# Optimization experiments

Measured on AMD Instinct MI355X. Metric: run time of the kernel, lower is better.

The kernel has to match this reference:

```python
import jax, jax.numpy as jnp
import numpy as np

L, D, H, G, HS, I, V, B, T = 4, 1024, 16, 4, 64, 2816, 32000, 4, 512
THETA = 10000.0
EPS = 1e-6


def setup_inputs() -> dict:
    key = jax.random.key(0)
    ks = jax.random.split(key, 10)
    s = 0.02
    return {
        "input_ids": jax.random.randint(ks[0], (B, T), 0, V),
        "embed": jax.random.normal(ks[1], (V, D)) * s,      # tied with lm_head
        "q_w": jax.random.normal(ks[2], (L, D, D)) * s,     # torch Linear: [out, in]
        "q_b": jax.random.normal(ks[3], (L, D)) * s,
        "kv_w": jax.random.normal(ks[4], (L, 2 * G * HS, D)) * s,
        "kv_b": jax.random.normal(ks[5], (L, 2 * G * HS)) * s,
        "o_w": jax.random.normal(ks[6], (L, D, D)) * s,
        "ln1_w": jnp.ones((L, D)),
        "ln2_w": jnp.ones((L, D)),
        "gate_w": jax.random.normal(ks[7], (L, I, D)) * s,
        "up_w": jax.random.normal(ks[8], (L, I, D)) * s,
        "down_w": jax.random.normal(ks[9], (L, D, I)) * s,
        "last_w": jnp.ones((D,)),
    }


def rms_norm(x, w):
    return x * jax.lax.rsqrt(jnp.mean(x * x, axis=-1, keepdims=True) + EPS) * w


def rope_tables(t, hs):
    inv_freq = 1.0 / (THETA ** (jnp.arange(0, hs, 2, dtype=jnp.float32) / hs))
    ang = jnp.arange(t, dtype=jnp.float32)[:, None] * inv_freq[None, :]  # [T, hs/2]
    emb = jnp.concatenate([ang, ang], axis=-1)                           # [T, hs]
    return jnp.cos(emb), jnp.sin(emb)


def rotate_half(x):
    x1, x2 = jnp.split(x, 2, axis=-1)
    return jnp.concatenate([-x2, x1], axis=-1)


def reference(input_ids, embed, q_w, q_b, kv_w, kv_b, o_w, ln1_w, ln2_w, gate_w, up_w, down_w, last_w):
    x = embed[input_ids]  # [B, T, D]
    cos, sin = rope_tables(T, HS)                    # [T, HS] (buffers, const)
    c, s_ = cos[None, None], sin[None, None]         # [1, 1, T, HS]
    causal = jnp.tril(jnp.ones((T, T), dtype=bool))
    scale = 1.0 / np.sqrt(HS).astype(np.float32)
    for l in range(L):
        h = rms_norm(x, ln1_w[l])
        q = (h @ q_w[l].T + q_b[l]).reshape(B, T, H, HS).transpose(0, 2, 1, 3)  # bhtd
        kv = h @ kv_w[l].T + kv_b[l]
        k, v = jnp.split(kv, 2, axis=-1)
        k = k.reshape(B, T, G, HS).transpose(0, 2, 1, 3)  # bgtd
        v = v.reshape(B, T, G, HS).transpose(0, 2, 1, 3)
        k = jnp.repeat(k, H // G, axis=1)  # GQA kv repeat -> bhtd
        v = jnp.repeat(v, H // G, axis=1)
        q = q * c + rotate_half(q) * s_
        k = k * c + rotate_half(k) * s_
        attn = jnp.einsum('bhtd,bhsd->bhts', q, k) * scale
        attn = jnp.where(causal, attn, -jnp.inf)
        attn = jax.nn.softmax(attn, axis=-1)
        o = jnp.einsum('bhts,bhsd->bhtd', attn, v).transpose(0, 2, 1, 3).reshape(B, T, D)
        x = x + o @ o_w[l].T  # o_proj has no bias
        h = rms_norm(x, ln2_w[l])
        x = x + (jax.nn.silu(h @ gate_w[l].T) * (h @ up_w[l].T)) @ down_w[l].T  # SwiGLU
    x = rms_norm(x, last_w)
    return x @ embed.T  # tied lm_head -> logits [B, T, V]
```

## Files before the change

kernel.cpp:

```cpp
#include <hip/hip_runtime.h>
#include <hip/hip_bf16.h>
#include <stdint.h>


typedef __bf16 bf16x8 __attribute__((ext_vector_type(8)));
typedef __bf16 bf16x4 __attribute__((ext_vector_type(4)));
typedef float  f32x4  __attribute__((ext_vector_type(4)));

#define AS1 __attribute__((address_space(1)))
#define AS3 __attribute__((address_space(3)))

__device__ __forceinline__ void gld_lds16(const void* g, void* l) {
  __builtin_amdgcn_global_load_lds((const AS1 void*)g, (AS3 void*)l, 16, 0, 0);
}

__device__ __forceinline__ void cvt4(const float* __restrict__ s, __bf16* __restrict__ d, int i) {
  f32x4 v = __builtin_nontemporal_load(&((const f32x4*)s)[i]);
  bf16x4 o;
#pragma unroll
  for (int j = 0; j < 4; ++j) o[j] = (__bf16)v[j];
  ((bf16x4*)d)[i] = o;
}

__global__ __launch_bounds__(256) void cvt_all(
    const float* __restrict__ e, __bf16* __restrict__ eb,
    const float* __restrict__ qw, __bf16* __restrict__ qwb,
    const float* __restrict__ kvw, __bf16* __restrict__ kvwb,
    const float* __restrict__ ow, __bf16* __restrict__ owb,
    const float* __restrict__ gw, __bf16* __restrict__ gwb,
    const float* __restrict__ uw, __bf16* __restrict__ uwb,
    const float* __restrict__ dw, __bf16* __restrict__ dwb) {
  const int C0 = 8192000;
  const int C1 = C0 + 1048576;
  const int C2 = C1 + 524288;
  const int C3 = C2 + 1048576;
  const int C4 = C3 + 2883584;
  const int C5 = C4 + 2883584;
  const int C6 = C5 + 2883584;
  for (int i = blockIdx.x * 256 + threadIdx.x; i < C6; i += gridDim.x * 256) {
    if (i < C0)      cvt4(e, eb, i);
    else if (i < C1) cvt4(qw, qwb, i - C0);
    else if (i < C2) cvt4(kvw, kvwb, i - C1);
    else if (i < C3) cvt4(ow, owb, i - C2);
    else if (i < C4) cvt4(gw, gwb, i - C3);
    else if (i < C5) cvt4(uw, uwb, i - C4);
    else             cvt4(dw, dwb, i - C5);
  }
}

__global__ __launch_bounds__(256) void embed_kernel(const int* __restrict__ ids,
                                                    const float* __restrict__ emb,
                                                    float* __restrict__ x) {
  const int tok = blockIdx.x;
  const float* src = emb + (size_t)ids[tok] * 1024;
  float* dst = x + (size_t)tok * 1024;
#pragma unroll
  for (int j = 0; j < 4; ++j) {
    const int d = threadIdx.x + j * 256;
    dst[d] = src[d];
  }
}

__global__ __launch_bounds__(256) void rmsnorm_kernel(const float* __restrict__ x,
                                                      const float* __restrict__ wgt,
                                                      __bf16* __restrict__ out) {
  const int row = blockIdx.x;
  const float* xr = x + (size_t)row * 1024;
  float v[4];
  float ss = 0.f;
#pragma unroll
  for (int j = 0; j < 4; ++j) { v[j] = xr[threadIdx.x + j * 256]; ss += v[j] * v[j]; }
#pragma unroll
  for (int m = 1; m < 64; m <<= 1) ss += __shfl_xor(ss, m, 64);
  __shared__ float red[4];
  if ((threadIdx.x & 63) == 0) red[threadIdx.x >> 6] = ss;
  __syncthreads();
  const float tot = red[0] + red[1] + red[2] + red[3];
  const float sc = rsqrtf(tot * (1.f / 1024.f) + 1e-6f);
#pragma unroll
  for (int j = 0; j < 4; ++j) {
    const int d = threadIdx.x + j * 256;
    out[(size_t)row * 1024 + d] = (__bf16)(v[j] * sc * wgt[d]);
  }
}

#define GEMM64_PRE                                                  \
  const int t = threadIdx.x;                                        \
  const int lane = t & 63;                                          \
  const int w = t >> 6, wr = w >> 1, wc = w & 1;                    \
  const int lr = lane & 15;                                         \
  const int lg = lane >> 4;                                         \
  const int sx = (lr & 7) << 4;                                     \
  int srow[4], scol[4];                                             \
  _Pragma("unroll") for (int j = 0; j < 4; ++j) {                   \
    const int q_ = (t + j * 256) * 16;                              \
    const int row_ = q_ >> 7;                                       \
    const int p_ = q_ ^ ((row_ & 7) << 4);                          \
    srow[j] = row_; scol[j] = (p_ & 127) >> 1;                      \
  }

#define STAGE64(base, Kd, ldsb, k0)                                 \
  _Pragma("unroll") for (int j = 0; j < 4; ++j)                     \
    gld_lds16((base) + (size_t)srow[j] * (Kd) + (k0) + scol[j],     \
              (char*)(ldsb) + (size_t)(t + j * 256) * 16);

#define GEMM64_FRAGS_MFMA                                           \
  bf16x8 af[4][2], bfr[4][2];                                       \
  _Pragma("unroll") for (int m = 0; m < 4; ++m)                     \
    _Pragma("unroll") for (int ks = 0; ks < 2; ++ks) {              \
      const int row_ = wr * 64 + m * 16 + lr;                       \
      af[m][ks] = *(const bf16x8*)((char*)As +                      \
          ((row_ * 128 + ks * 64 + lg * 16) ^ sx));                 \
    }                                                               \
  _Pragma("unroll") for (int n = 0; n < 4; ++n)                     \
    _Pragma("unroll") for (int ks = 0; ks < 2; ++ks) {              \
      const int row_ = wc * 64 + n * 16 + lr;                       \
      bfr[n][ks] = *(const bf16x8*)((char*)Bs +                     \
          ((row_ * 128 + ks * 64 + lg * 16) ^ sx));                 \
    }                                                               \
  _Pragma("unroll") for (int m = 0; m < 4; ++m)                     \
    _Pragma("unroll") for (int n = 0; n < 4; ++n)                   \
      _Pragma("unroll") for (int ks = 0; ks < 2; ++ks)              \
        acc[m][n] = __builtin_amdgcn_mfma_f32_16x16x32_bf16(        \
            af[m][ks], bfr[n][ks], acc[m][n], 0, 0, 0);

#define FLAT_SWZ(BMC, BNC)                                          \
  const int chunk_ = (int)(gridDim.x >> 3);                         \
  const int wg_ = (blockIdx.x & 7) * chunk_ + (blockIdx.x >> 3);    \
  const int bm = wg_ % (BMC);                                       \
  const int rest_ = wg_ / (BMC);                                    \
  const int bn = rest_ % (BNC);                                     \
  const int ks_ = rest_ / (BNC);                                    \
  (void)ks_;

__global__ __launch_bounds__(256) void oproj_gemm(const __bf16* __restrict__ A,
                                                  const __bf16* __restrict__ Bb,
                                                  float* __restrict__ Cf) {
  const int K = 1024;
  __shared__ __bf16 As[128 * 64];
  __shared__ __bf16 Bs[128 * 64];
  GEMM64_PRE
  FLAT_SWZ(16, 8)
  const int kbeg = ks_ * 256;

  const __bf16* a0 = A + (size_t)(bm * 128) * K;
  const __bf16* b0 = Bb + (size_t)(bn * 128) * K;

  f32x4 acc[4][4] = {};
  for (int k0 = kbeg; k0 < kbeg + 256; k0 += 64) {
    STAGE64(a0, K, As, k0)
    STAGE64(b0, K, Bs, k0)
    __syncthreads();
    GEMM64_FRAGS_MFMA
    __syncthreads();
  }
  const int r0 = bm * 128 + wr * 64 + lg * 4;
  const int c0 = bn * 128 + wc * 64 + lr;
#pragma unroll
  for (int m = 0; m < 4; ++m)
#pragma unroll
    for (int r = 0; r < 4; ++r) {
      const size_t rowoff = (size_t)(r0 + m * 16 + r) * 1024;
#pragma unroll
      for (int n = 0; n < 4; ++n) atomicAdd(&Cf[rowoff + c0 + n * 16], acc[m][n][r]);
    }
}

__global__ __launch_bounds__(256) void qkv_gemm(const __bf16* __restrict__ A,
                                                const __bf16* __restrict__ qw,
                                                const __bf16* __restrict__ kvw,
                                                const float* __restrict__ q_b,
                                                const float* __restrict__ kv_b,
                                                __bf16* __restrict__ qb,
                                                __bf16* __restrict__ kvb) {
  const int K = 1024;
  __shared__ __bf16 As[128 * 64];
  __shared__ __bf16 Bs[128 * 64];
  GEMM64_PRE
  FLAT_SWZ(16, 12)
  const bool isq = bn < 8;
  const int bnn = isq ? bn : bn - 8;
  const __bf16* Bw = (isq ? qw : kvw) + (size_t)(bnn * 128) * K;
  const __bf16* a0 = A + (size_t)(bm * 128) * K;

  f32x4 acc[4][4] = {};
  for (int k0 = 0; k0 < K; k0 += 64) {
    STAGE64(a0, K, As, k0)
    STAGE64(Bw, K, Bs, k0)
    __syncthreads();
    GEMM64_FRAGS_MFMA
    __syncthreads();
  }

  const int ldc = isq ? 1024 : 512;
  __bf16* out = isq ? qb : kvb;
  const float* bias = isq ? q_b : kv_b;
  const int cb = bnn * 128 + wc * 64;
  const bool dorope = isq || (cb < 256);
  float bv[4];
#pragma unroll
  for (int n = 0; n < 4; ++n) bv[n] = bias[cb + n * 16 + lr];
  float inv0 = __expf((float)lr * -0.28782313662425574f);
  float inv1 = __expf((float)(16 + lr) * -0.28782313662425574f);

  const int r0 = bm * 128 + wr * 64 + lg * 4;
#pragma unroll
  for (int m = 0; m < 4; ++m)
#pragma unroll
    for (int r = 0; r < 4; ++r) {
      const int row = r0 + m * 16 + r;
      float c4[4];
#pragma unroll
      for (int n = 0; n < 4; ++n) c4[n] = acc[m][n][r] + bv[n];
      if (dorope) {
        const float pos = (float)(row & 511);
        float sg, cg;
        __sincosf(pos * inv0, &sg, &cg);
        float x1 = c4[0], x2 = c4[2];
        c4[0] = x1 * cg - x2 * sg;
        c4[2] = x2 * cg + x1 * sg;
        __sincosf(pos * inv1, &sg, &cg);
        x1 = c4[1]; x2 = c4[3];
        c4[1] = x1 * cg - x2 * sg;
        c4[3] = x2 * cg + x1 * sg;
      }
      const size_t rowoff = (size_t)row * ldc;
#pragma unroll
      for (int n = 0; n < 4; ++n) out[rowoff + cb + n * 16 + lr] = (__bf16)c4[n];
    }
}

__global__ __launch_bounds__(256) void gateup_gemm(const __bf16* __restrict__ A,
                                                   const __bf16* __restrict__ gw,
                                                   const __bf16* __restrict__ uw,
                                                   __bf16* __restrict__ gbuf,
                                                   __bf16* __restrict__ ubuf) {
  const int K = 1024;
  __shared__ __bf16 As[128 * 64];
  __shared__ __bf16 Bs[128 * 64];
  GEMM64_PRE
  FLAT_SWZ(16, 44)
  const bool isg = bn < 22;
  const int bnn = isg ? bn : bn - 22;
  const __bf16* Bw = (isg ? gw : uw) + (size_t)(bnn * 128) * K;
  __bf16* out = isg ? gbuf : ubuf;
  const __bf16* a0 = A + (size_t)(bm * 128) * K;

  f32x4 acc[4][4] = {};
  for (int k0 = 0; k0 < K; k0 += 64) {
    STAGE64(a0, K, As, k0)
    STAGE64(Bw, K, Bs, k0)
    __syncthreads();
    GEMM64_FRAGS_MFMA
    __syncthreads();
  }
  const int r0 = bm * 128 + wr * 64 + lg * 4;
  const int c0 = bnn * 128 + wc * 64 + lr;
#pragma unroll
  for (int m = 0; m < 4; ++m)
#pragma unroll
    for (int r = 0; r < 4; ++r) {
      const size_t rowoff = (size_t)(r0 + m * 16 + r) * 2816;
#pragma unroll
      for (int n = 0; n < 4; ++n) out[rowoff + c0 + n * 16] = (__bf16)acc[m][n][r];
    }
}

#define GEMM_PREAMBLE32                                            \
  const int t = threadIdx.x;                                       \
  const int lane = t & 63;                                         \
  const int w = t >> 6, wr = w >> 1, wc = w & 1;                   \
  const int lr = lane & 15;                                        \
  const int lk = (lane >> 4) * 8;                                  \
  const int sr = t >> 2;                                           \
  const int scol = (t & 3) * 8;

__global__ __launch_bounds__(256) void down_gemm(const __bf16* __restrict__ g,
                                                 const __bf16* __restrict__ u,
                                                 const __bf16* __restrict__ Bb,
                                                 float* __restrict__ Cf) {
  const int K = 2816;
  __shared__ __bf16 As[128 * 32];
  __shared__ __bf16 Bs[128 * 32];
  GEMM_PREAMBLE32
  FLAT_SWZ(16, 8)
  const int klen = 704;
  const int kbeg = ks_ * klen;

  const size_t arow0 = (size_t)(bm * 128 + sr) * K + scol;
  const size_t arow1 = (size_t)(bm * 128 + 64 + sr) * K + scol;
  const __bf16* bb0 = Bb + (size_t)(bn * 128 + sr) * K + scol;
  const __bf16* bb1 = Bb + (size_t)(bn * 128 + 64 + sr) * K + scol;

  f32x4 acc[4][4] = {};
  for (int k0 = kbeg; k0 < kbeg + klen; k0 += 32) {
    {
      bf16x8 gv0 = *(const bf16x8*)(g + arow0 + k0);
      bf16x8 uv0 = *(const bf16x8*)(u + arow0 + k0);
      bf16x8 gv1 = *(const bf16x8*)(g + arow1 + k0);
      bf16x8 uv1 = *(const bf16x8*)(u + arow1 + k0);
      bf16x8 s0, s1;
#pragma unroll
      for (int j = 0; j < 8; ++j) {
        const float gf = (float)gv0[j];
        s0[j] = (__bf16)(gf / (1.f + __expf(-gf)) * (float)uv0[j]);
      }
#pragma unroll
      for (int j = 0; j < 8; ++j) {
        const float gf = (float)gv1[j];
        s1[j] = (__bf16)(gf / (1.f + __expf(-gf)) * (float)uv1[j]);
      }
      *(bf16x8*)&As[t * 8] = s0;
      *(bf16x8*)&As[2048 + t * 8] = s1;
    }
    gld_lds16(bb0 + k0, &Bs[t * 8]);
    gld_lds16(bb1 + k0, &Bs[2048 + t * 8]);
    __syncthreads();
    {
      bf16x8 af[4], bfr[4];
#pragma unroll
      for (int m = 0; m < 4; ++m) af[m] = *(const bf16x8*)&As[(wr * 64 + m * 16 + lr) * 32 + lk];
#pragma unroll
      for (int n = 0; n < 4; ++n) bfr[n] = *(const bf16x8*)&Bs[(wc * 64 + n * 16 + lr) * 32 + lk];
#pragma unroll
      for (int m = 0; m < 4; ++m)
#pragma unroll
        for (int n = 0; n < 4; ++n)
          acc[m][n] = __builtin_amdgcn_mfma_f32_16x16x32_bf16(af[m], bfr[n], acc[m][n], 0, 0, 0);
    }
    __syncthreads();
  }
  const int r0 = bm * 128 + wr * 64 + (lane >> 4) * 4;
  const int c0 = bn * 128 + wc * 64 + lr;
#pragma unroll
  for (int m = 0; m < 4; ++m)
#pragma unroll
    for (int r = 0; r < 4; ++r) {
      const size_t rowoff = (size_t)(r0 + m * 16 + r) * 1024;
#pragma unroll
      for (int n = 0; n < 4; ++n) atomicAdd(&Cf[rowoff + c0 + n * 16], acc[m][n][r]);
    }
}

__global__ __launch_bounds__(512, 2) void lmhead_gemm(const __bf16* __restrict__ A,
                                                      const __bf16* __restrict__ Bb,
                                                      float* __restrict__ C) {
  __shared__ __bf16 lds[2][4][8192];
  const int t = threadIdx.x;
  const int lane = t & 63;
  const int w = t >> 6;
  const int wr = w >> 2;
  const int wc = w & 3;
  const int lr = lane & 15;
  const int lg = lane >> 4;
  const int sx = (lr & 7) << 4;

  const int wg = (blockIdx.x & 7) * 125 + (blockIdx.x >> 3);
  const int bm = wg & 7;
  const int bn = wg >> 3;

  int srow[2], scol[2];
#pragma unroll
  for (int j = 0; j < 2; ++j) {
    const int q = (t + j * 512) * 16;
    const int row = q >> 7;
    const int p = q ^ ((row & 7) << 4);
    srow[j] = row;
    scol[j] = (p & 127) >> 1;
  }

  auto STAGE = [&](int buf, int kt) {
#pragma unroll
    for (int ht = 0; ht < 4; ++ht) {
      const __bf16* base = (ht < 2)
          ? A + (size_t)(bm * 256 + ht * 128) * 1024
          : Bb + (size_t)(bn * 256 + (ht - 2) * 128) * 1024;
#pragma unroll
      for (int j = 0; j < 2; ++j) {
        gld_lds16(base + (size_t)srow[j] * 1024 + kt * 64 + scol[j],
                  (char*)&lds[buf][ht][0] + (size_t)(t + j * 512) * 16);
      }
    }
  };

  STAGE(0, 0);
  STAGE(1, 1);

  f32x4 acc[8][4] = {};
  for (int kt = 0; kt < 16; ++kt) {
    const int cur = kt & 1;
    if (kt < 15) asm volatile("s_waitcnt vmcnt(8)" ::: "memory");
    else         asm volatile("s_waitcnt vmcnt(0)" ::: "memory");
    __builtin_amdgcn_s_barrier();

    const char* Ab = (const char*)&lds[cur][wr][0];
    const char* Bbs = (const char*)&lds[cur][2 + (wc >> 1)][0];
    const int rB0 = (wc & 1) * 64;

    bf16x8 af[8][2];
#pragma unroll
    for (int mi = 0; mi < 8; ++mi)
#pragma unroll
      for (int ksl = 0; ksl < 2; ++ksl) {
        const int row = mi * 16 + lr;
        af[mi][ksl] = *(const bf16x8*)(Ab + ((row * 128 + ksl * 64 + lg * 16) ^ sx));
      }
#pragma unroll
    for (int np = 0; np < 2; ++np) {
      bf16x8 bfr[2][2];
#pragma unroll
      for (int ni = 0; ni < 2; ++ni)
#pragma unroll
        for (int ksl = 0; ksl < 2; ++ksl) {
          const int row = rB0 + (np * 2 + ni) * 16 + lr;
          bfr[ni][ksl] = *(const bf16x8*)(Bbs + ((row * 128 + ksl * 64 + lg * 16) ^ sx));
        }
      __builtin_amdgcn_s_setprio(1);
#pragma unroll
      for (int mi = 0; mi < 8; ++mi)
#pragma unroll
        for (int ni = 0; ni < 2; ++ni)
#pragma unroll
          for (int ksl = 0; ksl < 2; ++ksl)
            acc[mi][np * 2 + ni] = __builtin_amdgcn_mfma_f32_16x16x32_bf16(
                af[mi][ksl], bfr[ni][ksl], acc[mi][np * 2 + ni], 0, 0, 0);
      __builtin_amdgcn_s_setprio(0);
    }
    asm volatile("s_waitcnt lgkmcnt(0)" ::: "memory");
    __builtin_amdgcn_s_barrier();
    if (kt + 2 < 16) STAGE(cur, kt + 2);
  }

  const int r0 = bm * 256 + wr * 128 + lg * 4;
  const int c0 = bn * 256 + wc * 64 + lr;
#pragma unroll
  for (int m = 0; m < 8; ++m)
#pragma unroll
    for (int r = 0; r < 4; ++r) {
      float* crow = C + (size_t)(r0 + m * 16 + r) * 32000 + c0;
#pragma unroll
      for (int n = 0; n < 4; ++n)
        __builtin_nontemporal_store(acc[m][n][r], crow + n * 16);
    }
}

__global__ __launch_bounds__(256) void attn_kernel(const __bf16* __restrict__ q,
                                                   const __bf16* __restrict__ kv,
                                                   __bf16* __restrict__ o) {
  const int qt = blockIdx.x, hh = blockIdx.y, b = blockIdx.z;
  const int g = hh >> 2;
  const int t = threadIdx.x, lane = t & 63, w = t >> 6;
  const int lr = lane & 15, lg = lane >> 4;

  __shared__ __bf16 Vt[64 * 72];
  __shared__ __bf16 Ps[64 * 72];

  bf16x8 qa[2];
  {
    const size_t qoff = ((size_t)(b * 512 + qt * 64 + w * 16 + lr)) * 1024 + hh * 64;
    qa[0] = *(const bf16x8*)(q + qoff + lg * 8);
    qa[1] = *(const bf16x8*)(q + qoff + 32 + lg * 8);
  }

  f32x4 acc_o[4] = {};
  float mrow[4], lrow[4];
#pragma unroll
  for (int r = 0; r < 4; ++r) { mrow[r] = -1e30f; lrow[r] = 0.f; }

  const int srow = t >> 3;
  const int sdv = (t & 7) * 8;

  for (int kt = 0; kt <= qt; ++kt) {
    const size_t krow = ((size_t)(b * 512 + kt * 64 + srow)) * 512;

    bf16x8 kb[4][2];
#pragma unroll
    for (int nf = 0; nf < 4; ++nf)
#pragma unroll
      for (int kc = 0; kc < 2; ++kc)
        kb[nf][kc] = *(const bf16x8*)(kv +
            ((size_t)(b * 512 + kt * 64 + nf * 16 + lr)) * 512 + g * 64 + kc * 32 + lg * 8);

    {
      const __bf16* vsrc = kv + krow + 256 + g * 64 + sdv;
      bf16x8 v0 = *(const bf16x8*)vsrc;
      bf16x8 v1 = *(const bf16x8*)(vsrc + 32 * 512);
#pragma unroll
      for (int j = 0; j < 8; ++j) Vt[(sdv + j) * 72 + srow] = v0[j];
#pragma unroll
      for (int j = 0; j < 8; ++j) Vt[(sdv + j) * 72 + srow + 32] = v1[j];
    }
    __syncthreads();

    f32x4 s[4] = {};
#pragma unroll
    for (int nf = 0; nf < 4; ++nf)
#pragma unroll
      for (int kc = 0; kc < 2; ++kc)
        s[nf] = __builtin_amdgcn_mfma_f32_16x16x32_bf16(qa[kc], kb[nf][kc], s[nf], 0, 0, 0);

    float pm[4][4], mx[4];
    const int qg = qt * 64 + w * 16 + lg * 4;
    const int kg = kt * 64 + lr;
#pragma unroll
    for (int r = 0; r < 4; ++r) mx[r] = -1e30f;
#pragma unroll
    for (int nf = 0; nf < 4; ++nf)
#pragma unroll
      for (int r = 0; r < 4; ++r) {
        float vv = s[nf][r] * 0.125f;
        vv = (kg + nf * 16 <= qg + r) ? vv : -1e30f;
        pm[nf][r] = vv;
        mx[r] = fmaxf(mx[r], vv);
      }
#pragma unroll
    for (int msk = 1; msk < 16; msk <<= 1)
#pragma unroll
      for (int r = 0; r < 4; ++r) mx[r] = fmaxf(mx[r], __shfl_xor(mx[r], msk, 64));

    float rs[4];
#pragma unroll
    for (int r = 0; r < 4; ++r) {
      const float mn = fmaxf(mrow[r], mx[r]);
      const float f = __expf(mrow[r] - mn);
      mrow[r] = mn;
      lrow[r] *= f;
#pragma unroll
      for (int df = 0; df < 4; ++df) acc_o[df][r] *= f;
      float rsum = 0.f;
#pragma unroll
      for (int nf = 0; nf < 4; ++nf) {
        const float pp = __expf(pm[nf][r] - mn);
        pm[nf][r] = pp;
        rsum += pp;
      }
      rs[r] = rsum;
    }
#pragma unroll
    for (int msk = 1; msk < 16; msk <<= 1)
#pragma unroll
      for (int r = 0; r < 4; ++r) rs[r] += __shfl_xor(rs[r], msk, 64);
#pragma unroll
    for (int r = 0; r < 4; ++r) lrow[r] += rs[r];

#pragma unroll
    for (int nf = 0; nf < 4; ++nf)
#pragma unroll
      for (int r = 0; r < 4; ++r)
        Ps[(w * 16 + lg * 4 + r) * 72 + nf * 16 + lr] = (__bf16)pm[nf][r];

#pragma unroll
    for (int df = 0; df < 4; ++df)
#pragma unroll
      for (int kc = 0; kc < 2; ++kc) {
        bf16x8 pa = *(const bf16x8*)&Ps[(w * 16 + lr) * 72 + kc * 32 + lg * 8];
        bf16x8 vb = *(const bf16x8*)&Vt[(df * 16 + lr) * 72 + kc * 32 + lg * 8];
        acc_o[df] = __builtin_amdgcn_mfma_f32_16x16x32_bf16(pa, vb, acc_o[df], 0, 0, 0);
      }
    __syncthreads();
  }

#pragma unroll
  for (int df = 0; df < 4; ++df)
#pragma unroll
    for (int r = 0; r < 4; ++r) {
      const int trow = qt * 64 + w * 16 + lg * 4 + r;
      o[((size_t)(b * 512 + trow)) * 1024 + hh * 64 + df * 16 + lr] =
          (__bf16)(acc_o[df][r] / lrow[r]);
    }
}

extern "C" void kernel_launch(void* const* d_in, const int* in_sizes, int n_in,
                              void* d_out, int out_size, void* d_ws, size_t ws_size,
                              hipStream_t stream) {
  const int* ids = (const int*)d_in[0];
  const float* emb_f = (const float*)d_in[1];
  const float* qw_f = (const float*)d_in[2];
  const float* q_b = (const float*)d_in[3];
  const float* kvw_f = (const float*)d_in[4];
  const float* kv_b = (const float*)d_in[5];
  const float* ow_f = (const float*)d_in[6];
  const float* ln1 = (const float*)d_in[7];
  const float* ln2 = (const float*)d_in[8];
  const float* gw_f = (const float*)d_in[9];
  const float* uw_f = (const float*)d_in[10];
  const float* dw_f = (const float*)d_in[11];
  const float* lw = (const float*)d_in[12];
  float* out = (float*)d_out;

  char* p = (char*)d_ws;
  float* x = (float*)p;        p += (size_t)2048 * 1024 * 4;
  __bf16* h = (__bf16*)p;      p += (size_t)2048 * 1024 * 2;
  __bf16* qb = (__bf16*)p;     p += (size_t)2048 * 1024 * 2;
  __bf16* kvb = (__bf16*)p;    p += (size_t)2048 * 512 * 2;
  __bf16* ao = (__bf16*)p;     p += (size_t)2048 * 1024 * 2;
  __bf16* gb = (__bf16*)p;     p += (size_t)2048 * 2816 * 2;
  __bf16* ub = (__bf16*)p;     p += (size_t)2048 * 2816 * 2;
  __bf16* emb_b = (__bf16*)p;  p += (size_t)32000 * 1024 * 2;
  __bf16* qw_b = (__bf16*)p;   p += (size_t)4 * 1024 * 1024 * 2;
  __bf16* kvw_b = (__bf16*)p;  p += (size_t)4 * 512 * 1024 * 2;
  __bf16* ow_b = (__bf16*)p;   p += (size_t)4 * 1024 * 1024 * 2;
  __bf16* gw_b = (__bf16*)p;   p += (size_t)4 * 2816 * 1024 * 2;
  __bf16* uw_b = (__bf16*)p;   p += (size_t)4 * 2816 * 1024 * 2;
  __bf16* dw_b = (__bf16*)p;   p += (size_t)4 * 2816 * 1024 * 2;

  cvt_all<<<4096, 256, 0, stream>>>(emb_f, emb_b, qw_f, qw_b, kvw_f, kvw_b,
                                    ow_f, ow_b, gw_f, gw_b, uw_f, uw_b, dw_f, dw_b);

  embed_kernel<<<2048, 256, 0, stream>>>(ids, emb_f, x);
  for (int l = 0; l < 4; ++l) {
    rmsnorm_kernel<<<2048, 256, 0, stream>>>(x, ln1 + l * 1024, h);
    qkv_gemm<<<192, 256, 0, stream>>>(
        h, qw_b + (size_t)l * 1024 * 1024, kvw_b + (size_t)l * 512 * 1024,
        q_b + l * 1024, kv_b + l * 512, qb, kvb);
    attn_kernel<<<dim3(8, 16, 4), 256, 0, stream>>>(qb, kvb, ao);
    oproj_gemm<<<512, 256, 0, stream>>>(ao, ow_b + (size_t)l * 1024 * 1024, x);
    rmsnorm_kernel<<<2048, 256, 0, stream>>>(x, ln2 + l * 1024, h);
    gateup_gemm<<<704, 256, 0, stream>>>(
        h, gw_b + (size_t)l * 2816 * 1024, uw_b + (size_t)l * 2816 * 1024, gb, ub);
    down_gemm<<<512, 256, 0, stream>>>(
        gb, ub, dw_b + (size_t)l * 1024 * 2816, x);
  }
  rmsnorm_kernel<<<2048, 256, 0, stream>>>(x, lw, h);
  lmhead_gemm<<<1000, 512, 0, stream>>>(h, emb_b, out);
}
```

Baseline: 996.8 us.

## Fuse embedding fp32-to-bf16 conversion into lm_head GEMM and prefetch attention K/V

The lm_head GEMM now reads the fp32 tied embedding directly into registers, converts it to bf16 and writes it to LDS. This replaces the separate conversion pass over the 32000x1024 table, which cost a full read plus a bf16 write. A1 and B are software-pipelined one tile ahead with a single LDS double buffer. The attention kernel also prefetches the next K/V tile into registers while computing the current one. In exchange, the lm_head B loads are twice as wide, each B tile is re-read by the 8 M-blocks in fp32, and the extra registers may reduce occupancy.

```diff
diff --git a/kernel.cpp b/kernel.cpp
--- a/kernel.cpp
+++ b/kernel.cpp
@@ -23,28 +23,25 @@
 }
 
 __global__ __launch_bounds__(256) void cvt_all(
-    const float* __restrict__ e, __bf16* __restrict__ eb,
     const float* __restrict__ qw, __bf16* __restrict__ qwb,
     const float* __restrict__ kvw, __bf16* __restrict__ kvwb,
     const float* __restrict__ ow, __bf16* __restrict__ owb,
     const float* __restrict__ gw, __bf16* __restrict__ gwb,
     const float* __restrict__ uw, __bf16* __restrict__ uwb,
     const float* __restrict__ dw, __bf16* __restrict__ dwb) {
-  const int C0 = 8192000;
-  const int C1 = C0 + 1048576;
-  const int C2 = C1 + 524288;
-  const int C3 = C2 + 1048576;
+  const int C0 = 1048576;
+  const int C1 = C0 + 524288;
+  const int C2 = C1 + 1048576;
+  const int C3 = C2 + 2883584;
   const int C4 = C3 + 2883584;
   const int C5 = C4 + 2883584;
-  const int C6 = C5 + 2883584;
-  for (int i = blockIdx.x * 256 + threadIdx.x; i < C6; i += gridDim.x * 256) {
-    if (i < C0)      cvt4(e, eb, i);
-    else if (i < C1) cvt4(qw, qwb, i - C0);
-    else if (i < C2) cvt4(kvw, kvwb, i - C1);
-    else if (i < C3) cvt4(ow, owb, i - C2);
-    else if (i < C4) cvt4(gw, gwb, i - C3);
-    else if (i < C5) cvt4(uw, uwb, i - C4);
-    else             cvt4(dw, dwb, i - C5);
+  for (int i = blockIdx.x * 256 + threadIdx.x; i < C5; i += gridDim.x * 256) {
+    if (i < C0)      cvt4(qw, qwb, i);
+    else if (i < C1) cvt4(kvw, kvwb, i - C0);
+    else if (i < C2) cvt4(ow, owb, i - C1);
+    else if (i < C3) cvt4(gw, gwb, i - C2);
+    else if (i < C4) cvt4(uw, uwb, i - C3);
+    else             cvt4(dw, dwb, i - C4);
   }
 }
 
@@ -343,7 +340,7 @@
 }
 
 __global__ __launch_bounds__(512, 2) void lmhead_gemm(const __bf16* __restrict__ A,
-                                                      const __bf16* __restrict__ Bb,
+                                                      const float* __restrict__ Bf,
                                                       float* __restrict__ C) {
   __shared__ __bf16 lds[2][4][8192];
   const int t = threadIdx.x;
@@ -369,29 +366,52 @@
     scol[j] = (p & 127) >> 1;
   }
 
-  auto STAGE = [&](int buf, int kt) {
-#pragma unroll
-    for (int ht = 0; ht < 4; ++ht) {
-      const __bf16* base = (ht < 2)
-          ? A + (size_t)(bm * 256 + ht * 128) * 1024
-          : Bb + (size_t)(bn * 256 + (ht - 2) * 128) * 1024;
+  auto STAGEA = [&](int buf, int kt) {
+#pragma unroll
+    for (int ht = 0; ht < 2; ++ht)
+#pragma unroll
+      for (int j = 0; j < 2; ++j)
+        gld_lds16(A + (size_t)(bm * 256 + ht * 128 + srow[j]) * 1024 + kt * 64 + scol[j],
+                  (char*)&lds[buf][ht][0] + (size_t)(t + j * 512) * 16);
+  };
+
+  f32x4 breg[2][2][2];
+  auto LOADB = [&](int kt) {
+#pragma unroll
+    for (int ht = 0; ht < 2; ++ht)
 #pragma unroll
       for (int j = 0; j < 2; ++j) {
-        gld_lds16(base + (size_t)srow[j] * 1024 + kt * 64 + scol[j],
-                  (char*)&lds[buf][ht][0] + (size_t)(t + j * 512) * 16);
-      }
-    }
+        const float* src = Bf + (size_t)(bn * 256 + ht * 128 + srow[j]) * 1024 + kt * 64 + scol[j];
+        breg[ht][j][0] = *(const f32x4*)src;
+        breg[ht][j][1] = *(const f32x4*)(src + 4);
+      }
   };
-
-  STAGE(0, 0);
-  STAGE(1, 1);
+  auto WRITEB = [&](int buf) {
+#pragma unroll
+    for (int ht = 0; ht < 2; ++ht)
+#pragma unroll
+      for (int j = 0; j < 2; ++j) {
+        bf16x8 o;
+#pragma unroll
+        for (int k = 0; k < 4; ++k) o[k] = (__bf16)breg[ht][j][0][k];
+#pragma unroll
+        for (int k = 0; k < 4; ++k) o[4 + k] = (__bf16)breg[ht][j][1][k];
+        *(bf16x8*)((char*)&lds[buf][2 + ht][0] + (size_t)(t + j * 512) * 16) = o;
+      }
+  };
+
+  LOADB(0);
+  STAGEA(0, 0);
+  WRITEB(0);
+  __syncthreads();
 
   f32x4 acc[8][4] = {};
   for (int kt = 0; kt < 16; ++kt) {
     const int cur = kt & 1;
-    if (kt < 15) asm volatile("s_waitcnt vmcnt(8)" ::: "memory");
-    else         asm volatile("s_waitcnt vmcnt(0)" ::: "memory");
-    __builtin_amdgcn_s_barrier();
+    if (kt < 15) {
+      LOADB(kt + 1);
+      STAGEA(cur ^ 1, kt + 1);
+    }
 
     const char* Ab = (const char*)&lds[cur][wr][0];
     const char* Bbs = (const char*)&lds[cur][2 + (wc >> 1)][0];
@@ -426,9 +446,9 @@
                 af[mi][ksl], bfr[ni][ksl], acc[mi][np * 2 + ni], 0, 0, 0);
       __builtin_amdgcn_s_setprio(0);
     }
-    asm volatile("s_waitcnt lgkmcnt(0)" ::: "memory");
-    __builtin_amdgcn_s_barrier();
-    if (kt + 2 < 16) STAGE(cur, kt + 2);
+
+    if (kt < 15) WRITEB(cur ^ 1);
+    __syncthreads();
   }
 
   const int r0 = bm * 256 + wr * 128 + lg * 4;
@@ -470,27 +490,29 @@
   const int srow = t >> 3;
   const int sdv = (t & 7) * 8;
 
+  bf16x8 kb[4][2], kb2[4][2], v0, v1, v0n, v1n;
+  auto LOADKV = [&](int kt, bf16x8 (&kbo)[4][2], bf16x8& va, bf16x8& vb2) {
+#pragma unroll
+    for (int nf = 0; nf < 4; ++nf)
+#pragma unroll
+      for (int kc = 0; kc < 2; ++kc)
+        kbo[nf][kc] = *(const bf16x8*)(kv +
+            ((size_t)(b * 512 + kt * 64 + nf * 16 + lr)) * 512 + g * 64 + kc * 32 + lg * 8);
+    const __bf16* vsrc = kv + ((size_t)(b * 512 + kt * 64 + srow)) * 512 + 256 + g * 64 + sdv;
+    va = *(const bf16x8*)vsrc;
+    vb2 = *(const bf16x8*)(vsrc + 32 * 512);
+  };
+
+  LOADKV(0, kb, v0, v1);
+
   for (int kt = 0; kt <= qt; ++kt) {
-    const size_t krow = ((size_t)(b * 512 + kt * 64 + srow)) * 512;
-
-    bf16x8 kb[4][2];
-#pragma unroll
-    for (int nf = 0; nf < 4; ++nf)
-#pragma unroll
-      for (int kc = 0; kc < 2; ++kc)
-        kb[nf][kc] = *(const bf16x8*)(kv +
-            ((size_t)(b * 512 + kt * 64 + nf * 16 + lr)) * 512 + g * 64 + kc * 32 + lg * 8);
-
-    {
-      const __bf16* vsrc = kv + krow + 256 + g * 64 + sdv;
-      bf16x8 v0 = *(const bf16x8*)vsrc;
-      bf16x8 v1 = *(const bf16x8*)(vsrc + 32 * 512);
-#pragma unroll
-      for (int j = 0; j < 8; ++j) Vt[(sdv + j) * 72 + srow] = v0[j];
-#pragma unroll
-      for (int j = 0; j < 8; ++j) Vt[(sdv + j) * 72 + srow + 32] = v1[j];
-    }
-    __syncthreads();
+#pragma unroll
+    for (int j = 0; j < 8; ++j) Vt[(sdv + j) * 72 + srow] = v0[j];
+#pragma unroll
+    for (int j = 0; j < 8; ++j) Vt[(sdv + j) * 72 + srow + 32] = v1[j];
+    __syncthreads();
+
+    if (kt < qt) LOADKV(kt + 1, kb2, v0n, v1n);
 
     f32x4 s[4] = {};
 #pragma unroll
@@ -558,6 +580,15 @@
         acc_o[df] = __builtin_amdgcn_mfma_f32_16x16x32_bf16(pa, vb, acc_o[df], 0, 0, 0);
       }
     __syncthreads();
+
+    if (kt < qt) {
+#pragma unroll
+      for (int nf = 0; nf < 4; ++nf)
+#pragma unroll
+        for (int kc = 0; kc < 2; ++kc) kb[nf][kc] = kb2[nf][kc];
+      v0 = v0n;
+      v1 = v1n;
+    }
   }
 
 #pragma unroll
@@ -596,7 +627,6 @@
   __bf16* ao = (__bf16*)p;     p += (size_t)2048 * 1024 * 2;
   __bf16* gb = (__bf16*)p;     p += (size_t)2048 * 2816 * 2;
   __bf16* ub = (__bf16*)p;     p += (size_t)2048 * 2816 * 2;
-  __bf16* emb_b = (__bf16*)p;  p += (size_t)32000 * 1024 * 2;
   __bf16* qw_b = (__bf16*)p;   p += (size_t)4 * 1024 * 1024 * 2;
   __bf16* kvw_b = (__bf16*)p;  p += (size_t)4 * 512 * 1024 * 2;
   __bf16* ow_b = (__bf16*)p;   p += (size_t)4 * 1024 * 1024 * 2;
@@ -604,8 +634,8 @@
   __bf16* uw_b = (__bf16*)p;   p += (size_t)4 * 2816 * 1024 * 2;
   __bf16* dw_b = (__bf16*)p;   p += (size_t)4 * 2816 * 1024 * 2;
 
-  cvt_all<<<4096, 256, 0, stream>>>(emb_f, emb_b, qw_f, qw_b, kvw_f, kvw_b,
-                                    ow_f, ow_b, gw_f, gw_b, uw_f, uw_b, dw_f, dw_b);
+  cvt_all<<<4096, 256, 0, stream>>>(qw_f, qw_b, kvw_f, kvw_b, ow_f, ow_b,
+                                    gw_f, gw_b, uw_f, uw_b, dw_f, dw_b);
 
   embed_kernel<<<2048, 256, 0, stream>>>(ids, emb_f, x);
   for (int l = 0; l < 4; ++l) {
@@ -622,5 +652,5 @@
         gb, ub, dw_b + (size_t)l * 1024 * 2816, x);
   }
   rmsnorm_kernel<<<2048, 256, 0, stream>>>(x, lw, h);
-  lmhead_gemm<<<1000, 512, 0, stream>>>(h, emb_b, out);
-}
+  lmhead_gemm<<<1000, 512, 0, stream>>>(h, emb_f, out);
+}
```

Result: slower. 1.149 ms (+15.2%).
